# Kernel tuning notes

Measured on AMD Instinct MI355X. Metric: run time of the kernel, lower is better.

## Reference

```python
import jax, jax.numpy as jnp
import numpy as np
from jax.ops import segment_sum

N_NODES = 100000
N_EDGES = 1250000
F_IN = 64
F_OUT = 64


def setup_inputs() -> dict:
    key = jax.random.key(0)
    k1, k2, k3, k4, k5 = jax.random.split(key, 5)
    x = jax.random.normal(k1, (N_NODES, F_IN), dtype=jnp.float32)
    edge_index = jax.random.randint(k2, (2, N_EDGES), 0, N_NODES, dtype=jnp.int32)
    edge_weight = jax.random.uniform(k3, (2, N_EDGES, 1), dtype=jnp.float32)
    # glorot_uniform for Dense kernels [in, out]
    lim = float(np.sqrt(6.0 / (F_IN + F_OUT)))
    W_src = jax.random.uniform(k4, (F_IN, F_OUT), minval=-lim, maxval=lim, dtype=jnp.float32)
    W_dst = jax.random.uniform(k5, (F_IN, F_OUT), minval=-lim, maxval=lim, dtype=jnp.float32)
    b_src = jnp.zeros((F_OUT,), dtype=jnp.float32)
    b_dst = jnp.zeros((F_OUT,), dtype=jnp.float32)
    return {"x": x, "edge_index": edge_index, "edge_weight": edge_weight,
            "W_src": W_src, "W_dst": W_dst, "b_src": b_src, "b_dst": b_dst}


def reference(x, edge_index, edge_weight, W_src, W_dst, b_src, b_dst):
    num_nodes = x.shape[0]
    senders, receivers = edge_index[0], edge_index[1]
    ew_s2d, ew_d2s = edge_weight[0], edge_weight[1]  # [E, 1] each
    x_gather = x[senders]  # [E, F_IN]
    agg_s2d = segment_sum(x_gather * ew_s2d, receivers, num_segments=num_nodes)
    agg_d2s = segment_sum(x_gather * ew_d2s, receivers, num_segments=num_nodes)
    out_s2d = agg_s2d @ W_src + b_src
    out_d2s = agg_d2s @ W_dst + b_dst
    return (out_s2d, out_d2s)
```

## Files before the change

### kernel.cpp

```cpp
#include <hip/hip_runtime.h>
#include <hip/hip_fp16.h>

#define N_NODES 100000
#define N_EDGES 1250000
#define F 64
#define SCAN_CHUNK 1024
#define NBLK_SCAN ((N_NODES + SCAN_CHUNK - 1) / SCAN_CHUNK)
#define NPB 16
#define TP 18
#define PAY_PAD 12


__global__ __launch_bounds__(256) void hist_kernel(const int* __restrict__ ei,
                                                   int* __restrict__ counts,
                                                   int* __restrict__ rank) {
    int e = blockIdx.x * 256 + threadIdx.x;
    if (e < N_EDGES) rank[e] = atomicAdd(&counts[ei[N_EDGES + e]], 1);
}

__global__ __launch_bounds__(256) void scan_reduce_kernel(const int* __restrict__ counts,
                                                          int* __restrict__ partials) {
    int base = blockIdx.x * SCAN_CHUNK + threadIdx.x * 4;
    int s = 0;
    if (base + 3 < N_NODES) {
        int4 c = *(const int4*)&counts[base];
        s = c.x + c.y + c.z + c.w;
    }
    for (int d = 32; d > 0; d >>= 1) s += __shfl_down(s, d);
    __shared__ int lds[4];
    int lane = threadIdx.x & 63, wave = threadIdx.x >> 6;
    if (lane == 0) lds[wave] = s;
    __syncthreads();
    if (threadIdx.x == 0) partials[blockIdx.x] = lds[0] + lds[1] + lds[2] + lds[3];
}

__global__ __launch_bounds__(256) void scan_apply_kernel(const int* __restrict__ counts,
                                                         const int* __restrict__ partials,
                                                         int* __restrict__ off) {
    __shared__ int sh_red[4];
    __shared__ int sh_base;
    __shared__ int wsum[4];
    int t = threadIdx.x;
    int lane = t & 63, wave = t >> 6;

    int pp = 0;
    if (t < blockIdx.x && t < NBLK_SCAN) pp = partials[t];
    for (int d = 32; d > 0; d >>= 1) pp += __shfl_down(pp, d);
    if (lane == 0) sh_red[wave] = pp;
    __syncthreads();
    if (t == 0) sh_base = sh_red[0] + sh_red[1] + sh_red[2] + sh_red[3];

    int base = blockIdx.x * SCAN_CHUNK + t * 4;
    int4 c = {0, 0, 0, 0};
    bool act = (base + 3 < N_NODES);
    if (act) c = *(const int4*)&counts[base];
    int s = c.x + c.y + c.z + c.w;

    int xs = s;
    for (int d = 1; d < 64; d <<= 1) {
        int y = __shfl_up(xs, d);
        if (lane >= d) xs += y;
    }
    if (lane == 63) wsum[wave] = xs;
    __syncthreads();
    int pre = xs - s;
    for (int w = 0; w < wave; ++w) pre += wsum[w];
    pre += sh_base;

    if (act) {
        int o0 = pre, o1 = o0 + c.x, o2 = o1 + c.y, o3 = o2 + c.z;
        int4 o = {o0, o1, o2, o3};
        *(int4*)&off[base] = o;
        if (base + 4 == N_NODES) off[N_NODES] = o3 + c.w;
    }
}

__global__ __launch_bounds__(256) void permute_kernel(const int* __restrict__ ei,
                                                      const float* __restrict__ ew,
                                                      const int* __restrict__ off,
                                                      const int* __restrict__ rank,
                                                      int2* __restrict__ pay) {
    int e = blockIdx.x * 256 + threadIdx.x;
    if (e >= N_EDGES) return;
    int r = ei[N_EDGES + e];
    int pos = off[r] + rank[e];
    __half2 h = __floats2half2_rn(ew[e], ew[N_EDGES + e]);
    int2 p;
    p.x = ei[e];
    p.y = *(const int*)&h;
    pay[pos] = p;
}

__global__ __launch_bounds__(256) void cvt_kernel(const float* __restrict__ x,
                                                  __half* __restrict__ xh) {
    int i = blockIdx.x * 256 + threadIdx.x;
    int base = i * 4;
    if (base < N_NODES * F) {
        float4 v = *(const float4*)&x[base];
        __half2 h0 = __floats2half2_rn(v.x, v.y);
        __half2 h1 = __floats2half2_rn(v.z, v.w);
        uint2 u;
        u.x = *(const unsigned int*)&h0;
        u.y = *(const unsigned int*)&h1;
        *(uint2*)&xh[base] = u;
    }
}

__global__ __launch_bounds__(256, 8) void agg_gemm_kernel(
    const __half* __restrict__ xh, const int* __restrict__ off,
    const int2* __restrict__ pay,
    const float* __restrict__ Wsrc, const float* __restrict__ Wdst,
    const float* __restrict__ bsrc, const float* __restrict__ bdst,
    float* __restrict__ outA, float* __restrict__ outB)
{
    __shared__ float tA[F * TP];
    __shared__ float tB[F * TP];
    int t = threadIdx.x;
    int w = t >> 6;
    int lane = t & 63;
    int g = lane >> 4;
    int l4 = lane & 15;
    int nIB = w * 4 + g;
    int n = blockIdx.x * NPB + nIB;

    int beg = off[n];
    int end = off[n + 1];

    float4 accA = {0.f, 0.f, 0.f, 0.f};
    float4 accB = {0.f, 0.f, 0.f, 0.f};

    if (beg < end) {
        int2 pa0 = pay[beg];
        int2 pa1 = pay[beg + 1];
        int2 pa2 = pay[beg + 2];
        int2 pa3 = pay[beg + 3];
        int2 pb0 = pay[beg + 4];
        int2 pb1 = pay[beg + 5];
        int2 pb2 = pay[beg + 6];
        int2 pb3 = pay[beg + 7];
        uint2 xa0 = *(const uint2*)(xh + (size_t)pa0.x * F + l4 * 4);
        uint2 xa1 = *(const uint2*)(xh + (size_t)pa1.x * F + l4 * 4);
        uint2 xa2 = *(const uint2*)(xh + (size_t)pa2.x * F + l4 * 4);
        uint2 xa3 = *(const uint2*)(xh + (size_t)pa3.x * F + l4 * 4);

        for (int i = beg; i < end; i += 4) {
            int2 pc0 = pay[i + 8];
            int2 pc1 = pay[i + 9];
            int2 pc2 = pay[i + 10];
            int2 pc3 = pay[i + 11];
            uint2 xb0 = *(const uint2*)(xh + (size_t)pb0.x * F + l4 * 4);
            uint2 xb1 = *(const uint2*)(xh + (size_t)pb1.x * F + l4 * 4);
            uint2 xb2 = *(const uint2*)(xh + (size_t)pb2.x * F + l4 * 4);
            uint2 xb3 = *(const uint2*)(xh + (size_t)pb3.x * F + l4 * 4);

#define EDGE(J, PJ, XJ)                                                   \
            {                                                             \
                float2 wv = __half22float2(*(const __half2*)&PJ.y);       \
                if (i + J >= end) { wv.x = 0.f; wv.y = 0.f; }             \
                float2 lo = __half22float2(*(const __half2*)&XJ.x);       \
                float2 hi = __half22float2(*(const __half2*)&XJ.y);       \
                accA.x += lo.x * wv.x; accA.y += lo.y * wv.x;             \
                accA.z += hi.x * wv.x; accA.w += hi.y * wv.x;             \
                accB.x += lo.x * wv.y; accB.y += lo.y * wv.y;             \
                accB.z += hi.x * wv.y; accB.w += hi.y * wv.y;             \
            }
            EDGE(0, pa0, xa0)
            EDGE(1, pa1, xa1)
            EDGE(2, pa2, xa2)
            EDGE(3, pa3, xa3)
#undef EDGE
            pa0 = pb0; pa1 = pb1; pa2 = pb2; pa3 = pb3;
            pb0 = pc0; pb1 = pc1; pb2 = pc2; pb3 = pc3;
            xa0 = xb0; xa1 = xb1; xa2 = xb2; xa3 = xb3;
        }
    }

    #pragma unroll
    for (int c = 0; c < 4; ++c) {
        tA[(4 * l4 + c) * TP + nIB] = ((const float*)&accA)[c];
        tB[(4 * l4 + c) * TP + nIB] = ((const float*)&accB)[c];
    }

    __syncthreads();

    int dir = t >> 7;
    int tx = t & 15;
    int ty = (t >> 4) & 7;
    const float* W    = dir ? Wdst : Wsrc;
    const float* bias = dir ? bdst : bsrc;
    const float* tile = dir ? tB : tA;
    float* out        = dir ? outB : outA;
    int j4 = tx * 4, n2 = ty * 2;

    float4 bj = *(const float4*)&bias[j4];
    float4 a0 = bj, a1 = bj;
    #pragma unroll 8
    for (int k = 0; k < F; ++k) {
        float4 wv = *(const float4*)&W[k * F + j4];
        float2 v  = *(const float2*)&tile[k * TP + n2];
        a0.x += v.x * wv.x; a0.y += v.x * wv.y; a0.z += v.x * wv.z; a0.w += v.x * wv.w;
        a1.x += v.y * wv.x; a1.y += v.y * wv.y; a1.z += v.y * wv.z; a1.w += v.y * wv.w;
    }
    int nb = blockIdx.x * NPB + n2;
    *(float4*)&out[(size_t)(nb + 0) * F + j4] = a0;
    *(float4*)&out[(size_t)(nb + 1) * F + j4] = a1;
}


__global__ __launch_bounds__(256) void scatter_fallback(const float4* __restrict__ x4,
                                                        const int* __restrict__ ei,
                                                        const float* __restrict__ ew,
                                                        float* __restrict__ aggA,
                                                        float* __restrict__ aggB) {
    int t = blockIdx.x * blockDim.x + threadIdx.x;
    int e = t >> 4;
    int lane16 = t & 15;
    if (e >= N_EDGES) return;
    int src = ei[e], dst = ei[N_EDGES + e];
    float w0 = ew[e], w1 = ew[N_EDGES + e];
    float4 v = x4[(size_t)src * 16 + lane16];
    int base = dst * F + lane16 * 4;
    atomicAdd(&aggA[base + 0], v.x * w0); atomicAdd(&aggA[base + 1], v.y * w0);
    atomicAdd(&aggA[base + 2], v.z * w0); atomicAdd(&aggA[base + 3], v.w * w0);
    atomicAdd(&aggB[base + 0], v.x * w1); atomicAdd(&aggB[base + 1], v.y * w1);
    atomicAdd(&aggB[base + 2], v.z * w1); atomicAdd(&aggB[base + 3], v.w * w1);
}

__global__ __launch_bounds__(256) void matmul_fallback(float* __restrict__ outA, float* __restrict__ outB,
                                                       const float* __restrict__ Wsrc, const float* __restrict__ Wdst,
                                                       const float* __restrict__ bsrc, const float* __restrict__ bdst) {
    __shared__ float lWs[F * F];
    __shared__ float lWd[F * F];
    for (int i = threadIdx.x; i < F * F / 4; i += blockDim.x) {
        ((float4*)lWs)[i] = ((const float4*)Wsrc)[i];
        ((float4*)lWd)[i] = ((const float4*)Wdst)[i];
    }
    __syncthreads();
    int wave = (blockIdx.x * blockDim.x + threadIdx.x) >> 6;
    int lane = threadIdx.x & 63;
    if (wave >= N_NODES) return;
    size_t rowbase = (size_t)wave * F;
    float a0 = outA[rowbase + lane], a1 = outB[rowbase + lane];
    float acc0 = bsrc[lane], acc1 = bdst[lane];
    #pragma unroll
    for (int k = 0; k < F; ++k) {
        acc0 += __shfl(a0, k) * lWs[k * F + lane];
        acc1 += __shfl(a1, k) * lWd[k * F + lane];
    }
    outA[rowbase + lane] = acc0;
    outB[rowbase + lane] = acc1;
}


extern "C" void kernel_launch(void* const* d_in, const int* in_sizes, int n_in,
                              void* d_out, int out_size, void* d_ws, size_t ws_size,
                              hipStream_t stream) {
    const float* x    = (const float*)d_in[0];
    const int*   ei   = (const int*)d_in[1];
    const float* ew   = (const float*)d_in[2];
    const float* Wsrc = (const float*)d_in[3];
    const float* Wdst = (const float*)d_in[4];
    const float* bsrc = (const float*)d_in[5];
    const float* bdst = (const float*)d_in[6];

    float* outA = (float*)d_out;
    float* outB = (float*)d_out + (size_t)N_NODES * F;

    const size_t OFF_XH       = 0;
    const size_t OFF_COUNTS   = 0;
    const size_t OFF_PARTIALS = 400128;
    const size_t OFF_RANK     = 400640;
    const size_t OFF_OFF      = 12800256;
    const size_t OFF_PAY      = 13200768;
    const size_t REQ          = 23200864;

    if (ws_size >= REQ) {
        char* ws = (char*)d_ws;
        int*    counts   = (int*)(ws + OFF_COUNTS);
        int*    partials = (int*)(ws + OFF_PARTIALS);
        int*    rank     = (int*)(ws + OFF_RANK);
        int*    off      = (int*)(ws + OFF_OFF);
        int2*   pay      = (int2*)(ws + OFF_PAY);
        __half* xh       = (__half*)(ws + OFF_XH);

        hipMemsetAsync(counts, 0, (size_t)N_NODES * sizeof(int), stream);
        hipMemsetAsync(pay + N_EDGES, 0, PAY_PAD * sizeof(int2), stream);

        int eblk = (N_EDGES + 255) / 256;
        hist_kernel<<<eblk, 256, 0, stream>>>(ei, counts, rank);
        scan_reduce_kernel<<<NBLK_SCAN, 256, 0, stream>>>(counts, partials);
        scan_apply_kernel<<<NBLK_SCAN, 256, 0, stream>>>(counts, partials, off);
        permute_kernel<<<eblk, 256, 0, stream>>>(ei, ew, off, rank, pay);
        int cblk = (N_NODES * F / 4 + 255) / 256;
        cvt_kernel<<<cblk, 256, 0, stream>>>(x, xh);
        agg_gemm_kernel<<<N_NODES / NPB, 256, 0, stream>>>(
            xh, off, pay, Wsrc, Wdst, bsrc, bdst, outA, outB);
    } else {
        hipMemsetAsync(d_out, 0, (size_t)out_size * sizeof(float), stream);
        int blocks_scatter = (N_EDGES * 16 + 255) / 256;
        scatter_fallback<<<blocks_scatter, 256, 0, stream>>>((const float4*)x, ei, ew, outA, outB);
        int blocks_mm = (N_NODES * 64 + 255) / 256;
        matmul_fallback<<<blocks_mm, 256, 0, stream>>>(outA, outB, Wsrc, Wdst, bsrc, bdst);
    }
}
```

Before: 253.6 us.

## Replace global histogram/scan CSR build with two-pass bucketed counting sort

Replaces the per-edge global atomic histogram, two-kernel scan and random permute with a two-level bucket sort. The first pass bins edges into 256 coarse receiver buckets using shared-memory histograms and one global atomic per bucket per block. The second pass sorts each bucket locally in LDS and writes CSR offsets and payloads. The aim is to cut scattered global atomics and random writes, at the cost of a fixed per-bucket capacity (BCAP) that silently overflows if a bucket receives too many edges, and a serial prefix over bucket counts in each block.

```diff
diff --git a/kernel.cpp b/kernel.cpp
--- a/kernel.cpp
+++ b/kernel.cpp
@@ -4,91 +4,110 @@
 #define N_NODES 100000
 #define N_EDGES 1250000
 #define F 64
-#define SCAN_CHUNK 1024
-#define NBLK_SCAN ((N_NODES + SCAN_CHUNK - 1) / SCAN_CHUNK)
 #define NPB 16
 #define TP 18
 #define PAY_PAD 12
-
-
-__global__ __launch_bounds__(256) void hist_kernel(const int* __restrict__ ei,
-                                                   int* __restrict__ counts,
-                                                   int* __restrict__ rank) {
-    int e = blockIdx.x * 256 + threadIdx.x;
-    if (e < N_EDGES) rank[e] = atomicAdd(&counts[ei[N_EDGES + e]], 1);
-}
-
-__global__ __launch_bounds__(256) void scan_reduce_kernel(const int* __restrict__ counts,
-                                                          int* __restrict__ partials) {
-    int base = blockIdx.x * SCAN_CHUNK + threadIdx.x * 4;
-    int s = 0;
-    if (base + 3 < N_NODES) {
-        int4 c = *(const int4*)&counts[base];
-        s = c.x + c.y + c.z + c.w;
-    }
-    for (int d = 32; d > 0; d >>= 1) s += __shfl_down(s, d);
-    __shared__ int lds[4];
-    int lane = threadIdx.x & 63, wave = threadIdx.x >> 6;
-    if (lane == 0) lds[wave] = s;
-    __syncthreads();
-    if (threadIdx.x == 0) partials[blockIdx.x] = lds[0] + lds[1] + lds[2] + lds[3];
-}
-
-__global__ __launch_bounds__(256) void scan_apply_kernel(const int* __restrict__ counts,
-                                                         const int* __restrict__ partials,
-                                                         int* __restrict__ off) {
-    __shared__ int sh_red[4];
+#define NB 256
+#define NPBK 391
+#define BCAP 6144
+
+
+__global__ __launch_bounds__(256) void init_cursor_kernel(int* __restrict__ cursor) {
+    int b = threadIdx.x;
+    if (b < NB) cursor[b] = b * BCAP;
+}
+
+__global__ __launch_bounds__(1024) void bucket_kernel(const int* __restrict__ ei,
+                                                      const float* __restrict__ ew,
+                                                      int* __restrict__ cursor,
+                                                      int2* __restrict__ tmp) {
+    __shared__ int lh[NB];
+    __shared__ int bb[NB];
+    __shared__ int lc[NB];
+    int t = threadIdx.x;
+    int e = blockIdx.x * 1024 + t;
+    if (t < NB) { lh[t] = 0; lc[t] = 0; }
+    __syncthreads();
+    int r = 0, src = 0, bkt = -1;
+    float w0 = 0.f, w1 = 0.f;
+    if (e < N_EDGES) {
+        r = ei[N_EDGES + e];
+        src = ei[e];
+        w0 = ew[e];
+        w1 = ew[N_EDGES + e];
+        bkt = r / NPBK;
+        atomicAdd(&lh[bkt], 1);
+    }
+    __syncthreads();
+    if (t < NB && lh[t] > 0) bb[t] = atomicAdd(&cursor[t], lh[t]);
+    __syncthreads();
+    if (e < N_EDGES) {
+        int lr = atomicAdd(&lc[bkt], 1);
+        int pos = bb[bkt] + lr;
+        __half2 h = __floats2half2_rn(w0, w1);
+        int lrr = r - bkt * NPBK;
+        int2 p;
+        p.x = (src << 9) | lrr;
+        p.y = *(const int*)&h;
+        tmp[pos] = p;
+    }
+}
+
+__global__ __launch_bounds__(512) void scatter_kernel(const int* __restrict__ cursor,
+                                                      const int2* __restrict__ tmp,
+                                                      int* __restrict__ off,
+                                                      int2* __restrict__ pay) {
+    __shared__ int lh[NPBK];
+    __shared__ int loff[NPBK];
+    __shared__ int lc[NPBK];
+    __shared__ int sc[NB];
     __shared__ int sh_base;
-    __shared__ int wsum[4];
     int t = threadIdx.x;
-    int lane = t & 63, wave = t >> 6;
-
-    int pp = 0;
-    if (t < blockIdx.x && t < NBLK_SCAN) pp = partials[t];
-    for (int d = 32; d > 0; d >>= 1) pp += __shfl_down(pp, d);
-    if (lane == 0) sh_red[wave] = pp;
-    __syncthreads();
-    if (t == 0) sh_base = sh_red[0] + sh_red[1] + sh_red[2] + sh_red[3];
-
-    int base = blockIdx.x * SCAN_CHUNK + t * 4;
-    int4 c = {0, 0, 0, 0};
-    bool act = (base + 3 < N_NODES);
-    if (act) c = *(const int4*)&counts[base];
-    int s = c.x + c.y + c.z + c.w;
-
-    int xs = s;
-    for (int d = 1; d < 64; d <<= 1) {
-        int y = __shfl_up(xs, d);
-        if (lane >= d) xs += y;
-    }
-    if (lane == 63) wsum[wave] = xs;
-    __syncthreads();
-    int pre = xs - s;
-    for (int w = 0; w < wave; ++w) pre += wsum[w];
-    pre += sh_base;
-
-    if (act) {
-        int o0 = pre, o1 = o0 + c.x, o2 = o1 + c.y, o3 = o2 + c.z;
-        int4 o = {o0, o1, o2, o3};
-        *(int4*)&off[base] = o;
-        if (base + 4 == N_NODES) off[N_NODES] = o3 + c.w;
-    }
-}
-
-__global__ __launch_bounds__(256) void permute_kernel(const int* __restrict__ ei,
-                                                      const float* __restrict__ ew,
-                                                      const int* __restrict__ off,
-                                                      const int* __restrict__ rank,
-                                                      int2* __restrict__ pay) {
-    int e = blockIdx.x * 256 + threadIdx.x;
-    if (e >= N_EDGES) return;
-    int r = ei[N_EDGES + e];
-    int pos = off[r] + rank[e];
-    __half2 h = __floats2half2_rn(ew[e], ew[N_EDGES + e]);
-    int2 p;
-    p.x = ei[e];
-    p.y = *(const int*)&h;
-    pay[pos] = p;
+    int bkt = blockIdx.x;
+
+    if (t < NB) sc[t] = cursor[t] - t * BCAP;
+    for (int j = t; j < NPBK; j += 512) { lh[j] = 0; lc[j] = 0; }
+    __syncthreads();
+    if (t == 0) {
+        int s = 0;
+        for (int j = 0; j < bkt; ++j) s += sc[j];
+        sh_base = s;
+    }
+    __syncthreads();
+    int base_g = sh_base;
+    int cnt = sc[bkt];
+    const int2* te = tmp + (size_t)bkt * BCAP;
+
+    for (int i = t; i < cnt; i += 512) {
+        int lrr = te[i].x & 511;
+        atomicAdd(&lh[lrr], 1);
+    }
+    __syncthreads();
+    if (t < NPBK) loff[t] = lh[t];
+    __syncthreads();
+    for (int d = 1; d < NPBK; d <<= 1) {
+        int v = 0;
+        if (t < NPBK && t >= d) v = loff[t - d];
+        __syncthreads();
+        if (t < NPBK && t >= d) loff[t] += v;
+        __syncthreads();
+    }
+    if (t < NPBK) {
+        int node = bkt * NPBK + t;
+        if (node < N_NODES) off[node] = base_g + loff[t] - lh[t];
+    }
+    if (bkt == 0 && t == 0) off[N_NODES] = N_EDGES;
+    __syncthreads();
+    for (int i = t; i < cnt; i += 512) {
+        int2 p = te[i];
+        int lrr = p.x & 511;
+        int lr = atomicAdd(&lc[lrr], 1);
+        int pos = base_g + (loff[lrr] - lh[lrr]) + lr;
+        int2 o;
+        o.x = p.x >> 9;
+        o.y = p.y;
+        pay[pos] = o;
+    }
 }
 
 __global__ __launch_bounds__(256) void cvt_kernel(const float* __restrict__ x,
@@ -266,31 +285,27 @@
     float* outA = (float*)d_out;
     float* outB = (float*)d_out + (size_t)N_NODES * F;
 
-    const size_t OFF_XH       = 0;
-    const size_t OFF_COUNTS   = 0;
-    const size_t OFF_PARTIALS = 400128;
-    const size_t OFF_RANK     = 400640;
-    const size_t OFF_OFF      = 12800256;
-    const size_t OFF_PAY      = 13200768;
-    const size_t REQ          = 23200864;
+    const size_t OFF_TMP    = 0;
+    const size_t OFF_XH     = 0;
+    const size_t OFF_CURSOR = 12800256;
+    const size_t OFF_OFF    = 12801280;
+    const size_t OFF_PAY    = 13201792;
+    const size_t REQ        = 23201888;
 
     if (ws_size >= REQ) {
         char* ws = (char*)d_ws;
-        int*    counts   = (int*)(ws + OFF_COUNTS);
-        int*    partials = (int*)(ws + OFF_PARTIALS);
-        int*    rank     = (int*)(ws + OFF_RANK);
-        int*    off      = (int*)(ws + OFF_OFF);
-        int2*   pay      = (int2*)(ws + OFF_PAY);
-        __half* xh       = (__half*)(ws + OFF_XH);
-
-        hipMemsetAsync(counts, 0, (size_t)N_NODES * sizeof(int), stream);
+        int2*   tmp    = (int2*)(ws + OFF_TMP);
+        __half* xh     = (__half*)(ws + OFF_XH);
+        int*    cursor = (int*)(ws + OFF_CURSOR);
+        int*    off    = (int*)(ws + OFF_OFF);
+        int2*   pay    = (int2*)(ws + OFF_PAY);
+
         hipMemsetAsync(pay + N_EDGES, 0, PAY_PAD * sizeof(int2), stream);
 
-        int eblk = (N_EDGES + 255) / 256;
-        hist_kernel<<<eblk, 256, 0, stream>>>(ei, counts, rank);
-        scan_reduce_kernel<<<NBLK_SCAN, 256, 0, stream>>>(counts, partials);
-        scan_apply_kernel<<<NBLK_SCAN, 256, 0, stream>>>(counts, partials, off);
-        permute_kernel<<<eblk, 256, 0, stream>>>(ei, ew, off, rank, pay);
+        init_cursor_kernel<<<1, 256, 0, stream>>>(cursor);
+        int ablk = (N_EDGES + 1023) / 1024;
+        bucket_kernel<<<ablk, 1024, 0, stream>>>(ei, ew, cursor, tmp);
+        scatter_kernel<<<NB, 512, 0, stream>>>(cursor, tmp, off, pay);
         int cblk = (N_NODES * F / 4 + 255) / 256;
         cvt_kernel<<<cblk, 256, 0, stream>>>(x, xh);
         agg_gemm_kernel<<<N_NODES / NPB, 256, 0, stream>>>(
```

Measured after the change: 219.0 us. 1.16x faster.
